# Performance work log

Hardware: AMD Instinct MI355X
Metric: run time of the kernel (lower is better)

The kernel has to match this reference:

```python
import jax, jax.numpy as jnp
import numpy as np

B, S, D = 2, 2048, 1024
H, HD = 16, 64  # H*HD == D (required by proj layer)
SCALE = D ** -0.5  # NOTE: original scales by full input dim (x.shape[-1]), not head dim


def setup_inputs() -> dict:
    key = jax.random.key(0)
    ks = jax.random.split(key, 7)
    std = D ** -0.5
    x = jax.random.normal(ks[0], (B, S, D), dtype=jnp.float32)
    # per-head projection weights, stacked: [H, D, HD] so x @ Wq[h] == Linear(D->HD)
    Wq = jax.random.normal(ks[1], (H, D, HD), dtype=jnp.float32) * std
    Wk = jax.random.normal(ks[2], (H, D, HD), dtype=jnp.float32) * std
    Wv = jax.random.normal(ks[3], (H, D, HD), dtype=jnp.float32) * std
    # output projection Linear(D, D) with bias
    Wp = jax.random.normal(ks[4], (D, D), dtype=jnp.float32) * std
    bp = jax.random.normal(ks[5], (D,), dtype=jnp.float32) * 0.01
    return {"x": x, "Wq": Wq, "Wk": Wk, "Wv": Wv, "Wp": Wp, "bp": bp}


def reference(x, Wq, Wk, Wv, Wp, bp):
    # All heads see the full x (atsp=False path). Dropout in eval mode (identity).
    q = jnp.einsum('bsd,hde->bhse', x, Wq)  # [B,H,S,HD]
    k = jnp.einsum('bsd,hde->bhse', x, Wk)
    v = jnp.einsum('bsd,hde->bhse', x, Wv)
    scores = jnp.einsum('bhse,bhte->bhst', q, k) * SCALE  # [B,H,S,S]
    causal = jnp.tril(jnp.ones((S, S), dtype=bool))
    scores = jnp.where(causal, scores, -jnp.inf)
    attn = jax.nn.softmax(scores, axis=-1)
    out = jnp.einsum('bhst,bhte->bhse', attn, v)          # [B,H,S,HD]
    # concat heads along last dim in head order: [B,S,H*HD]
    out = out.transpose(0, 2, 1, 3).reshape(B, S, H * HD)
    return out @ Wp.T + bp
```

## Files before the change

kernel.cpp:

```cpp
#include <hip/hip_runtime.h>

typedef __bf16 bf16x8 __attribute__((ext_vector_type(8)));
typedef __bf16 bf16x4 __attribute__((ext_vector_type(4)));
typedef float f32x4 __attribute__((ext_vector_type(4)));
typedef unsigned short u16;
typedef unsigned int u32;

static constexpr int kS = 2048, kD = 1024, kHD = 64;
static constexpr float kQScale = 0.03125f * 1.44269504f;

__device__ __forceinline__ u16 f2bf(float f) {
  union { float f; u32 u; } v; v.f = f;
  u32 r = v.u + 0x7FFFu + ((v.u >> 16) & 1u);
  return (u16)(r >> 16);
}
__device__ __forceinline__ float bf2f(u16 u) {
  union { u32 u; float f; } v; v.u = ((u32)u) << 16;
  return v.f;
}
__device__ __forceinline__ u32 pk2(float a, float b) {
  return (u32)f2bf(a) | ((u32)f2bf(b) << 16);
}
__device__ __forceinline__ f32x4 mfma16(bf16x8 a, bf16x8 b, f32x4 c) {
  return __builtin_amdgcn_mfma_f32_16x16x32_bf16(a, b, c, 0, 0, 0);
}
__device__ __forceinline__ void gld16(u16* lds, const u16* g) {
  __builtin_amdgcn_global_load_lds(
      (const __attribute__((address_space(1))) u32*)g,
      (__attribute__((address_space(3))) u32*)lds, 16, 0, 0);
}

__device__ __forceinline__ bool probe_f32(const u16* __restrict__ xr) {
  int ex = (xr[threadIdx.x] >> 7) & 0xFF;
  int n = __syncthreads_count(ex >= 134);
  return n > 8;
}

union Pack8 { u16 u[8]; uint4 v; };

__global__ void cast_all_kernel(const void* Wq, const void* Wk, const void* Wv,
                                const void* Wp, const void* x,
                                u16* __restrict__ Wt, u16* __restrict__ Wpb,
                                u16* __restrict__ xb) {
  bool f32m = probe_f32((const u16*)x);
  int bid = blockIdx.x;
  int t = threadIdx.x;
  __shared__ float Ts[64][65];
  if (bid < 768) {
    int u = bid >> 4;
    int d0 = (bid & 15) * 64;
    int w = u >> 4, h = u & 15;
    const void* srcv = (w == 0) ? Wq : (w == 1) ? Wk : Wv;
    const float* sf = (const float*)srcv + (size_t)h * kD * kHD;
    const u16*   sb = (const u16*)srcv + (size_t)h * kD * kHD;
    int row = t >> 4;
    int c4 = (t & 15) * 4;
    for (int rr = 0; rr < 64; rr += 16) {
      int r = rr + row;
      if (f32m) {
        float4 v = *(const float4*)&sf[(size_t)(d0 + r) * kHD + c4];
        Ts[r][c4 + 0] = v.x; Ts[r][c4 + 1] = v.y; Ts[r][c4 + 2] = v.z; Ts[r][c4 + 3] = v.w;
      } else {
        const u16* p = &sb[(size_t)(d0 + r) * kHD + c4];
        Ts[r][c4 + 0] = bf2f(p[0]); Ts[r][c4 + 1] = bf2f(p[1]);
        Ts[r][c4 + 2] = bf2f(p[2]); Ts[r][c4 + 3] = bf2f(p[3]);
      }
    }
    __syncthreads();
    for (int rr = 0; rr < 64; rr += 16) {
      int e = rr + row;
      uint2 pk;
      pk.x = pk2(Ts[c4 + 0][e], Ts[c4 + 1][e]);
      pk.y = pk2(Ts[c4 + 2][e], Ts[c4 + 3][e]);
      *(uint2*)&Wt[(size_t)u * (kHD * kD) + (size_t)e * kD + d0 + c4] = pk;
    }
  } else if (bid < 1792) {
    if (!f32m) return;
    int i = ((bid - 768) * 256 + t) * 4;
    float4 v = *(const float4*)((const float*)Wp + i);
    uint2 pk; pk.x = pk2(v.x, v.y); pk.y = pk2(v.z, v.w);
    *(uint2*)&Wpb[i] = pk;
  } else {
    if (!f32m) return;
    size_t i = ((size_t)(bid - 1792) * 256 + t) * 8;
    const float* xf = (const float*)x;
    float4 a = *(const float4*)&xf[i];
    float4 b = *(const float4*)&xf[i + 4];
    Pack8 pk;
    pk.u[0] = f2bf(a.x); pk.u[1] = f2bf(a.y); pk.u[2] = f2bf(a.z); pk.u[3] = f2bf(a.w);
    pk.u[4] = f2bf(b.x); pk.u[5] = f2bf(b.y); pk.u[6] = f2bf(b.z); pk.u[7] = f2bf(b.w);
    *(uint4*)&xb[i] = pk.v;
  }
}

__global__ __launch_bounds__(256) void qkv_gemm_kernel(const u16* __restrict__ xb,
    const u16* __restrict__ Wt, u16* __restrict__ Q, u16* __restrict__ K,
    u16* __restrict__ Vt, const void* __restrict__ x) {
  bool f32m = probe_f32((const u16*)x);
  const u16* xsrc = f32m ? xb : (const u16*)x;
  int m0 = blockIdx.x * 128;
  int n0 = blockIdx.y * 128;
  int w = (int)(blockIdx.y >> 3);
  const u16 *Ap, *Bp; int a0, b0;
  if (w == 2) { Ap = xsrc; a0 = m0; Bp = Wt; b0 = n0; }
  else        { Ap = Wt; a0 = n0; Bp = xsrc; b0 = m0; }
  int t = threadIdx.x;
  int wv = t >> 6, l = t & 63;
  int fr = l & 15, fq = l >> 4;
  int wI = (wv >> 1) * 64, wJ = (wv & 1) * 64;
  __shared__ __align__(16) u16 As[128][64];
  __shared__ __align__(16) u16 Bs[128][64];
  int srow = l >> 3;
  int scol = (((l & 7) ^ srow)) * 8;
  int dcol = (l & 7) * 8;
  int sw = fr & 7;
  f32x4 acc[4][4];
#pragma unroll
  for (int ii = 0; ii < 4; ++ii)
#pragma unroll
    for (int jj = 0; jj < 4; ++jj)
      for (int i = 0; i < 4; ++i) acc[ii][jj][i] = 0.f;

  for (int kb = 0; kb < kD / 64; ++kb) {
    int k0 = kb * 64;
    __syncthreads();
#pragma unroll
    for (int j = 0; j < 4; ++j) {
      int row = (wv * 4 + j) * 8 + srow;
      gld16(&As[row][dcol], &Ap[(size_t)(a0 + row) * kD + k0 + scol]);
      gld16(&Bs[row][dcol], &Bp[(size_t)(b0 + row) * kD + k0 + scol]);
    }
    __syncthreads();
    bf16x8 af[4][2], bg[4][2];
#pragma unroll
    for (int ii = 0; ii < 4; ++ii) {
      af[ii][0] = *(const bf16x8*)&As[wI + ii * 16 + fr][((0 + fq) ^ sw) * 8];
      af[ii][1] = *(const bf16x8*)&As[wI + ii * 16 + fr][((4 + fq) ^ sw) * 8];
    }
#pragma unroll
    for (int jj = 0; jj < 4; ++jj) {
      bg[jj][0] = *(const bf16x8*)&Bs[wJ + jj * 16 + fr][((0 + fq) ^ sw) * 8];
      bg[jj][1] = *(const bf16x8*)&Bs[wJ + jj * 16 + fr][((4 + fq) ^ sw) * 8];
    }
#pragma unroll
    for (int ii = 0; ii < 4; ++ii)
#pragma unroll
      for (int jj = 0; jj < 4; ++jj) {
        acc[ii][jj] = mfma16(af[ii][0], bg[jj][0], acc[ii][jj]);
        acc[ii][jj] = mfma16(af[ii][1], bg[jj][1], acc[ii][jj]);
      }
  }

  if (w == 2) {
    int uh = wv & 1;
    int u = 2 * blockIdx.y + uh;
    int h = u & 15;
#pragma unroll
    for (int jj = 0; jj < 4; ++jj) {
      int e = jj * 16 + fr;
#pragma unroll
      for (int ii = 0; ii < 4; ++ii) {
        int m = m0 + wI + ii * 16 + fq * 4;
        int b = m >> 11, s0 = m & 2047;
        int bh = b * 16 + h;
        *(bf16x4*)&Vt[((size_t)bh * kHD + e) * kS + s0] =
            __builtin_convertvector(acc[ii][jj], bf16x4);
      }
    }
  } else {
    int uh = wv >> 1;
    int u = 2 * blockIdx.y + uh;
    int h = u & 15;
    bool isQ = (w == 0);
    u16* dst = isQ ? Q : K;
#pragma unroll
    for (int jj = 0; jj < 4; ++jj) {
      int m = m0 + wJ + jj * 16 + fr;
      int b = m >> 11, s = m & 2047;
      int bh = b * 16 + h;
      size_t rowb = ((size_t)bh * kS + s) * kHD;
#pragma unroll
      for (int ii = 0; ii < 4; ++ii) {
        int e0 = ii * 16 + fq * 4;
        f32x4 v = acc[ii][jj];
        if (isQ) v *= kQScale;
        *(bf16x4*)&dst[rowb + e0] = __builtin_convertvector(v, bf16x4);
      }
    }
  }
}

static __device__ const signed char kQtab[48] = {
  15,31,30,31,
  14,29,28,30,29,
  13,27,26,28,27,
  12,25,24,26,25,
  11,23,22,24,23,
  10,21,20,22,21,
   9,19,18,20,19,
   8,17,16,18,17,
   7,16,
   6,5,4,3,2,1,0};
static __device__ const signed char kPtab[48] = {
  2,0,0,1,
  2,0,0,1,1,
  2,0,0,1,1,
  2,0,0,1,1,
  2,0,0,1,1,
  2,0,0,1,1,
  2,0,0,1,1,
  2,0,0,1,1,
  2,1,
  2,2,2,2,2,2,2};

__global__ __launch_bounds__(256) void attn_kernel(const u16* __restrict__ Q,
    const u16* __restrict__ K, const u16* __restrict__ Vt, u16* __restrict__ cat,
    float* __restrict__ Po, float* __restrict__ Pl, int split) {
  int bh = (int)(blockIdx.x & 31);
  int c  = (int)(blockIdx.x >> 5);
  int qb, part;
  if (split) { qb = kQtab[c]; part = kPtab[c]; }
  else       { qb = 31 - c;   part = 2; }
  int h0 = (qb + 2) >> 1;
  int tbeg = (part == 1) ? h0 : 0;
  int tend = (part == 0) ? h0 - 1 : qb;
  int q0 = qb * 64;
  int t = threadIdx.x;
  int wv = t >> 6, l = t & 63;
  int fr = l & 15, fq = l >> 4;
  __shared__ __align__(16) u16 Ks[64][64];
  __shared__ __align__(16) u16 Vs[64][64];
  __shared__ __align__(16) u16 Ps[4][16][64];
  const u16* Qb = Q + (size_t)bh * kS * kHD;
  const u16* Kb = K + (size_t)bh * kS * kHD;
  const u16* Vb = Vt + (size_t)bh * kHD * kS;

  int qrow = q0 + wv * 16 + fr;
  bf16x8 qf0 = *(const bf16x8*)&Qb[(size_t)qrow * kHD + fq * 8];
  bf16x8 qf1 = *(const bf16x8*)&Qb[(size_t)qrow * kHD + 32 + fq * 8];

  f32x4 O[4];
#pragma unroll
  for (int nt = 0; nt < 4; ++nt) for (int i = 0; i < 4; ++i) O[nt][i] = 0.f;
  float lsum = 0.f;

  int jr = l >> 3;
  int dcol = (l & 7) * 8;
  int scol = ((l & 7) ^ jr) * 8;
  int r0 = wv * 16 + jr;
  int r1 = r0 + 8;
  int sw = fr & 7;

  {
    int tb = tbeg * 64;
    gld16(&Ks[r0][dcol], &Kb[(size_t)(tb + r0) * kHD + scol]);
    gld16(&Ks[r1][dcol], &Kb[(size_t)(tb + r1) * kHD + scol]);
    gld16(&Vs[r0][dcol], &Vb[(size_t)r0 * kS + tb + scol]);
    gld16(&Vs[r1][dcol], &Vb[(size_t)r1 * kS + tb + scol]);
  }
  __syncthreads();

  for (int tt = tbeg; tt <= tend; ++tt) {
    int t0 = tt * 64;
    f32x4 sc[4];
    __builtin_amdgcn_s_setprio(1);
#pragma unroll
    for (int nt = 0; nt < 4; ++nt) {
      f32x4 z; z[0] = z[1] = z[2] = z[3] = 0.f;
      bf16x8 a0 = *(const bf16x8*)&Ks[nt * 16 + fr][((0 + fq) ^ sw) * 8];
      bf16x8 a1 = *(const bf16x8*)&Ks[nt * 16 + fr][((4 + fq) ^ sw) * 8];
      z = mfma16(a0, qf0, z);
      z = mfma16(a1, qf1, z);
      sc[nt] = z;
    }
    __builtin_amdgcn_s_setprio(0);
    if (tt == qb) {
#pragma unroll
      for (int nt = 0; nt < 4; ++nt)
#pragma unroll
        for (int r = 0; r < 4; ++r)
          if (t0 + nt * 16 + fq * 4 + r > qrow) sc[nt][r] = -__builtin_inff();
    }
#pragma unroll
    for (int nt = 0; nt < 4; ++nt) {
#pragma unroll
      for (int r = 0; r < 4; ++r) {
        float p = exp2f(sc[nt][r]);
        sc[nt][r] = p;
        lsum += p;
      }
      *(bf16x4*)&Ps[wv][fr][(((nt * 2 + (fq >> 1)) ^ sw) * 8) + (fq & 1) * 4] =
          __builtin_convertvector(sc[nt], bf16x4);
    }
    bf16x8 pf0 = *(const bf16x8*)&Ps[wv][fr][(fq ^ sw) * 8];
    bf16x8 pf1 = *(const bf16x8*)&Ps[wv][fr][((4 + fq) ^ sw) * 8];
    __builtin_amdgcn_s_setprio(1);
#pragma unroll
    for (int nt = 0; nt < 4; ++nt) {
      bf16x8 v0 = *(const bf16x8*)&Vs[nt * 16 + fr][((0 + fq) ^ sw) * 8];
      bf16x8 v1 = *(const bf16x8*)&Vs[nt * 16 + fr][((4 + fq) ^ sw) * 8];
      O[nt] = mfma16(v0, pf0, O[nt]);
      O[nt] = mfma16(v1, pf1, O[nt]);
    }
    __builtin_amdgcn_s_setprio(0);
    if (tt < tend) {
      __syncthreads();
      int t0n = t0 + 64;
      gld16(&Ks[r0][dcol], &Kb[(size_t)(t0n + r0) * kHD + scol]);
      gld16(&Ks[r1][dcol], &Kb[(size_t)(t0n + r1) * kHD + scol]);
      gld16(&Vs[r0][dcol], &Vb[(size_t)r0 * kS + t0n + scol]);
      gld16(&Vs[r1][dcol], &Vb[(size_t)r1 * kS + t0n + scol]);
      __syncthreads();
    }
  }
  lsum += __shfl_xor(lsum, 16, 64);
  lsum += __shfl_xor(lsum, 32, 64);
  if (part == 2) {
    float inv = 1.0f / lsum;
    int b = bh >> 4, h = bh & 15;
    size_t rowbase = ((size_t)(b * kS + qrow)) * kD + h * kHD;
#pragma unroll
    for (int nt = 0; nt < 4; ++nt) {
      f32x4 ov = O[nt] * inv;
      *(bf16x4*)&cat[rowbase + nt * 16 + fq * 4] = __builtin_convertvector(ov, bf16x4);
    }
  } else {
    int slot = ((bh << 4) + (qb - 16)) * 2 + part;
    float* Pb = Po + (size_t)slot * 4096 + (wv * 16 + fr) * 64;
    if (fq == 0) Pl[slot * 64 + wv * 16 + fr] = lsum;
#pragma unroll
    for (int nt = 0; nt < 4; ++nt)
      *(f32x4*)&Pb[nt * 16 + fq * 4] = O[nt];
  }
}

__global__ __launch_bounds__(256) void attn_combine_kernel(
    const float* __restrict__ Po, const float* __restrict__ Pl,
    u16* __restrict__ cat) {
  int bh = (int)(blockIdx.x >> 4);
  int lvl = (int)(blockIdx.x & 15);
  int t = threadIdx.x;
  int slot = ((bh << 4) + lvl) * 2;
  int b = bh >> 4, h = bh & 15;
  int e0 = (t & 15) * 4;
  for (int qq = 0; qq < 64; qq += 16) {
    int q = qq + (t >> 4);
    const float* A = Po + (size_t)slot * 4096 + q * 64 + e0;
    float l = Pl[slot * 64 + q] + Pl[(slot + 1) * 64 + q];
    float inv = 1.0f / l;
    f32x4 a = *(const f32x4*)A;
    f32x4 bv = *(const f32x4*)(A + 4096);
    f32x4 v = (a + bv) * inv;
    int qrow = (lvl + 16) * 64 + q;
    *(bf16x4*)&cat[((size_t)(b * kS + qrow)) * kD + h * kHD + e0] =
        __builtin_convertvector(v, bf16x4);
  }
}

__global__ __launch_bounds__(256) void out_gemm_kernel(const u16* __restrict__ cat,
    const u16* __restrict__ Wpb, const void* __restrict__ Wp,
    const void* __restrict__ bp, void* __restrict__ out,
    const void* __restrict__ x) {
  bool f32m = probe_f32((const u16*)x);
  const u16* wsrc = f32m ? Wpb : (const u16*)Wp;
  int m0 = blockIdx.x * 64;
  int n0 = blockIdx.y * 128;
  int t = threadIdx.x;
  int wv = t >> 6, l = t & 63;
  int fr = l & 15, fq = l >> 4;
  int wI = (wv >> 1) * 64, wJ = (wv & 1) * 32;
  __shared__ __align__(16) u16 As[128][64];
  __shared__ __align__(16) u16 Bs[64][64];
  int srow = l >> 3;
  int scol = (((l & 7) ^ srow)) * 8;
  int dcol = (l & 7) * 8;
  int sw = fr & 7;
  f32x4 acc[4][2];
#pragma unroll
  for (int ii = 0; ii < 4; ++ii)
#pragma unroll
    for (int jj = 0; jj < 2; ++jj)
      for (int i = 0; i < 4; ++i) acc[ii][jj][i] = 0.f;

  for (int kb = 0; kb < kD / 64; ++kb) {
    int k0 = kb * 64;
    __syncthreads();
#pragma unroll
    for (int j = 0; j < 4; ++j) {
      int row = j * 32 + wv * 8 + srow;
      gld16(&As[row][dcol], &wsrc[(size_t)(n0 + row) * kD + k0 + scol]);
    }
#pragma unroll
    for (int j = 0; j < 2; ++j) {
      int row = j * 32 + wv * 8 + srow;
      gld16(&Bs[row][dcol], &cat[(size_t)(m0 + row) * kD + k0 + scol]);
    }
    __syncthreads();
    bf16x8 af[4][2], bg[2][2];
#pragma unroll
    for (int ii = 0; ii < 4; ++ii) {
      af[ii][0] = *(const bf16x8*)&As[wI + ii * 16 + fr][((0 + fq) ^ sw) * 8];
      af[ii][1] = *(const bf16x8*)&As[wI + ii * 16 + fr][((4 + fq) ^ sw) * 8];
    }
#pragma unroll
    for (int jj = 0; jj < 2; ++jj) {
      bg[jj][0] = *(const bf16x8*)&Bs[wJ + jj * 16 + fr][((0 + fq) ^ sw) * 8];
      bg[jj][1] = *(const bf16x8*)&Bs[wJ + jj * 16 + fr][((4 + fq) ^ sw) * 8];
    }
#pragma unroll
    for (int ii = 0; ii < 4; ++ii)
#pragma unroll
      for (int jj = 0; jj < 2; ++jj) {
        acc[ii][jj] = mfma16(af[ii][0], bg[jj][0], acc[ii][jj]);
        acc[ii][jj] = mfma16(af[ii][1], bg[jj][1], acc[ii][jj]);
      }
  }
  const float* bpf = (const float*)bp;
  const u16*   bpb = (const u16*)bp;
#pragma unroll
  for (int ii = 0; ii < 4; ++ii) {
    int n = n0 + wI + ii * 16 + fq * 4;
    f32x4 bias;
    if (f32m) bias = *(const f32x4*)&bpf[n];
    else { bias[0] = bf2f(bpb[n]); bias[1] = bf2f(bpb[n + 1]);
           bias[2] = bf2f(bpb[n + 2]); bias[3] = bf2f(bpb[n + 3]); }
#pragma unroll
    for (int jj = 0; jj < 2; ++jj) {
      int m = m0 + wJ + jj * 16 + fr;
      f32x4 v = acc[ii][jj] + bias;
      if (f32m) *(f32x4*)&((float*)out)[(size_t)m * kD + n] = v;
      else      *(bf16x4*)&((u16*)out)[(size_t)m * kD + n] = __builtin_convertvector(v, bf16x4);
    }
  }
}

extern "C" void kernel_launch(void* const* d_in, const int* in_sizes, int n_in,
                              void* d_out, int out_size, void* d_ws, size_t ws_size,
                              hipStream_t stream) {
  const void* x  = d_in[0];
  const void* Wq = d_in[1];
  const void* Wk = d_in[2];
  const void* Wv = d_in[3];
  const void* Wp = d_in[4];
  const void* bp = d_in[5];

  char* ws = (char*)d_ws;
  u16* Wt  = (u16*)(ws + 256);
  u16* Wpb = (u16*)(ws + 256 + 6291456);
  u16* Qp  = (u16*)(ws + 256 + 6291456 + 2097152);
  u16* Kp  = Qp  + (size_t)32 * 2048 * 64;
  u16* Vtp = Kp  + (size_t)32 * 2048 * 64;
  u16* xb  = Vtp + (size_t)32 * 2048 * 64;
  u16* cat = xb;
  size_t poOff = 256 + 6291456 + 2097152 + (size_t)4 * 8388608;
  size_t plOff = poOff + (size_t)32 * 16 * 2 * 4096 * 4;
  size_t needWs = plOff + (size_t)32 * 16 * 2 * 64 * 4;
  int split = (ws_size >= needWs) ? 1 : 0;
  float* Po = (float*)(ws + poOff);
  float* Pl = (float*)(ws + plOff);

  cast_all_kernel<<<3840, 256, 0, stream>>>(Wq, Wk, Wv, Wp, x, Wt, Wpb, xb);
  qkv_gemm_kernel<<<dim3(32, 24), 256, 0, stream>>>(xb, Wt, Qp, Kp, Vtp, x);
  attn_kernel<<<split ? 1536 : 1024, 256, 0, stream>>>(Qp, Kp, Vtp, cat, Po, Pl, split);
  if (split)
    attn_combine_kernel<<<512, 256, 0, stream>>>(Po, Pl, cat);
  out_gemm_kernel<<<dim3(64, 8), 256, 0, stream>>>(cat, Wpb, Wp, bp, d_out, x);
}
```

Baseline: 181.1 us.

## Process two query sub-tiles per wave in attention with 128-thread blocks

Restructures the attention kernel so each of 2 waves handles 32 query rows (two 16-row groups) instead of 4 waves handling 16 rows each. Each K/V fragment loaded from shared memory is reused across both query groups, halving LDS reads per MFMA, and each thread issues twice as many global loads to fill the tiles. The trade-off is fewer waves per block to hide latency, roughly double the accumulator registers per thread, and lower per-block parallelism.

Measured after the change: 186.2 us. +2.8%, slower.

```diff
diff --git a/kernel.cpp b/kernel.cpp
--- a/kernel.cpp
+++ b/kernel.cpp
@@ -213,7 +213,7 @@
   2,1,
   2,2,2,2,2,2,2};
 
-__global__ __launch_bounds__(256) void attn_kernel(const u16* __restrict__ Q,
+__global__ __launch_bounds__(128) void attn_kernel(const u16* __restrict__ Q,
     const u16* __restrict__ K, const u16* __restrict__ Vt, u16* __restrict__ cat,
     float* __restrict__ Po, float* __restrict__ Pl, int split) {
   int bh = (int)(blockIdx.x & 31);
@@ -230,107 +230,141 @@
   int fr = l & 15, fq = l >> 4;
   __shared__ __align__(16) u16 Ks[64][64];
   __shared__ __align__(16) u16 Vs[64][64];
-  __shared__ __align__(16) u16 Ps[4][16][64];
+  __shared__ __align__(16) u16 Ps[2][2][16][64];
   const u16* Qb = Q + (size_t)bh * kS * kHD;
   const u16* Kb = K + (size_t)bh * kS * kHD;
   const u16* Vb = Vt + (size_t)bh * kHD * kS;
 
-  int qrow = q0 + wv * 16 + fr;
-  bf16x8 qf0 = *(const bf16x8*)&Qb[(size_t)qrow * kHD + fq * 8];
-  bf16x8 qf1 = *(const bf16x8*)&Qb[(size_t)qrow * kHD + 32 + fq * 8];
-
-  f32x4 O[4];
-#pragma unroll
-  for (int nt = 0; nt < 4; ++nt) for (int i = 0; i < 4; ++i) O[nt][i] = 0.f;
-  float lsum = 0.f;
-
-  int jr = l >> 3;
-  int dcol = (l & 7) * 8;
-  int scol = ((l & 7) ^ jr) * 8;
-  int r0 = wv * 16 + jr;
-  int r1 = r0 + 8;
+  int qrow[2];
+  bf16x8 qf[2][2];
+#pragma unroll
+  for (int g = 0; g < 2; ++g) {
+    qrow[g] = q0 + wv * 32 + g * 16 + fr;
+    qf[g][0] = *(const bf16x8*)&Qb[(size_t)qrow[g] * kHD + fq * 8];
+    qf[g][1] = *(const bf16x8*)&Qb[(size_t)qrow[g] * kHD + 32 + fq * 8];
+  }
+
+  f32x4 O[2][4];
+#pragma unroll
+  for (int g = 0; g < 2; ++g)
+#pragma unroll
+    for (int nt = 0; nt < 4; ++nt)
+      for (int i = 0; i < 4; ++i) O[g][nt][i] = 0.f;
+  float lsum[2] = {0.f, 0.f};
+
+  int jr = t >> 3;
+  int dcol = (t & 7) * 8;
+  int scol = ((t & 7) ^ (jr & 7)) * 8;
   int sw = fr & 7;
 
   {
     int tb = tbeg * 64;
-    gld16(&Ks[r0][dcol], &Kb[(size_t)(tb + r0) * kHD + scol]);
-    gld16(&Ks[r1][dcol], &Kb[(size_t)(tb + r1) * kHD + scol]);
-    gld16(&Vs[r0][dcol], &Vb[(size_t)r0 * kS + tb + scol]);
-    gld16(&Vs[r1][dcol], &Vb[(size_t)r1 * kS + tb + scol]);
+#pragma unroll
+    for (int k = 0; k < 4; ++k) {
+      int r = jr + k * 16;
+      gld16(&Ks[r][dcol], &Kb[(size_t)(tb + r) * kHD + scol]);
+      gld16(&Vs[r][dcol], &Vb[(size_t)r * kS + tb + scol]);
+    }
   }
   __syncthreads();
 
   for (int tt = tbeg; tt <= tend; ++tt) {
     int t0 = tt * 64;
-    f32x4 sc[4];
+    f32x4 sc[2][4];
     __builtin_amdgcn_s_setprio(1);
 #pragma unroll
     for (int nt = 0; nt < 4; ++nt) {
-      f32x4 z; z[0] = z[1] = z[2] = z[3] = 0.f;
       bf16x8 a0 = *(const bf16x8*)&Ks[nt * 16 + fr][((0 + fq) ^ sw) * 8];
       bf16x8 a1 = *(const bf16x8*)&Ks[nt * 16 + fr][((4 + fq) ^ sw) * 8];
-      z = mfma16(a0, qf0, z);
-      z = mfma16(a1, qf1, z);
-      sc[nt] = z;
+#pragma unroll
+      for (int g = 0; g < 2; ++g) {
+        f32x4 z; z[0] = z[1] = z[2] = z[3] = 0.f;
+        z = mfma16(a0, qf[g][0], z);
+        z = mfma16(a1, qf[g][1], z);
+        sc[g][nt] = z;
+      }
     }
     __builtin_amdgcn_s_setprio(0);
     if (tt == qb) {
 #pragma unroll
-      for (int nt = 0; nt < 4; ++nt)
-#pragma unroll
-        for (int r = 0; r < 4; ++r)
-          if (t0 + nt * 16 + fq * 4 + r > qrow) sc[nt][r] = -__builtin_inff();
-    }
-#pragma unroll
-    for (int nt = 0; nt < 4; ++nt) {
-#pragma unroll
-      for (int r = 0; r < 4; ++r) {
-        float p = exp2f(sc[nt][r]);
-        sc[nt][r] = p;
-        lsum += p;
-      }
-      *(bf16x4*)&Ps[wv][fr][(((nt * 2 + (fq >> 1)) ^ sw) * 8) + (fq & 1) * 4] =
-          __builtin_convertvector(sc[nt], bf16x4);
-    }
-    bf16x8 pf0 = *(const bf16x8*)&Ps[wv][fr][(fq ^ sw) * 8];
-    bf16x8 pf1 = *(const bf16x8*)&Ps[wv][fr][((4 + fq) ^ sw) * 8];
+      for (int g = 0; g < 2; ++g)
+#pragma unroll
+        for (int nt = 0; nt < 4; ++nt)
+#pragma unroll
+          for (int r = 0; r < 4; ++r)
+            if (t0 + nt * 16 + fq * 4 + r > qrow[g]) sc[g][nt][r] = -__builtin_inff();
+    }
+#pragma unroll
+    for (int g = 0; g < 2; ++g)
+#pragma unroll
+      for (int nt = 0; nt < 4; ++nt) {
+#pragma unroll
+        for (int r = 0; r < 4; ++r) {
+          float p = exp2f(sc[g][nt][r]);
+          sc[g][nt][r] = p;
+          lsum[g] += p;
+        }
+        *(bf16x4*)&Ps[wv][g][fr][(((nt * 2 + (fq >> 1)) ^ sw) * 8) + (fq & 1) * 4] =
+            __builtin_convertvector(sc[g][nt], bf16x4);
+      }
+    bf16x8 pf[2][2];
+#pragma unroll
+    for (int g = 0; g < 2; ++g) {
+      pf[g][0] = *(const bf16x8*)&Ps[wv][g][fr][(fq ^ sw) * 8];
+      pf[g][1] = *(const bf16x8*)&Ps[wv][g][fr][((4 + fq) ^ sw) * 8];
+    }
     __builtin_amdgcn_s_setprio(1);
 #pragma unroll
     for (int nt = 0; nt < 4; ++nt) {
       bf16x8 v0 = *(const bf16x8*)&Vs[nt * 16 + fr][((0 + fq) ^ sw) * 8];
       bf16x8 v1 = *(const bf16x8*)&Vs[nt * 16 + fr][((4 + fq) ^ sw) * 8];
-      O[nt] = mfma16(v0, pf0, O[nt]);
-      O[nt] = mfma16(v1, pf1, O[nt]);
+#pragma unroll
+      for (int g = 0; g < 2; ++g) {
+        O[g][nt] = mfma16(v0, pf[g][0], O[g][nt]);
+        O[g][nt] = mfma16(v1, pf[g][1], O[g][nt]);
+      }
     }
     __builtin_amdgcn_s_setprio(0);
     if (tt < tend) {
       __syncthreads();
       int t0n = t0 + 64;
-      gld16(&Ks[r0][dcol], &Kb[(size_t)(t0n + r0) * kHD + scol]);
-      gld16(&Ks[r1][dcol], &Kb[(size_t)(t0n + r1) * kHD + scol]);
-      gld16(&Vs[r0][dcol], &Vb[(size_t)r0 * kS + t0n + scol]);
-      gld16(&Vs[r1][dcol], &Vb[(size_t)r1 * kS + t0n + scol]);
+#pragma unroll
+      for (int k = 0; k < 4; ++k) {
+        int r = jr + k * 16;
+        gld16(&Ks[r][dcol], &Kb[(size_t)(t0n + r) * kHD + scol]);
+        gld16(&Vs[r][dcol], &Vb[(size_t)r * kS + t0n + scol]);
+      }
       __syncthreads();
     }
   }
-  lsum += __shfl_xor(lsum, 16, 64);
-  lsum += __shfl_xor(lsum, 32, 64);
+#pragma unroll
+  for (int g = 0; g < 2; ++g) {
+    lsum[g] += __shfl_xor(lsum[g], 16, 64);
+    lsum[g] += __shfl_xor(lsum[g], 32, 64);
+  }
   if (part == 2) {
-    float inv = 1.0f / lsum;
     int b = bh >> 4, h = bh & 15;
-    size_t rowbase = ((size_t)(b * kS + qrow)) * kD + h * kHD;
-#pragma unroll
-    for (int nt = 0; nt < 4; ++nt) {
-      f32x4 ov = O[nt] * inv;
-      *(bf16x4*)&cat[rowbase + nt * 16 + fq * 4] = __builtin_convertvector(ov, bf16x4);
+#pragma unroll
+    for (int g = 0; g < 2; ++g) {
+      float inv = 1.0f / lsum[g];
+      size_t rowbase = ((size_t)(b * kS + qrow[g])) * kD + h * kHD;
+#pragma unroll
+      for (int nt = 0; nt < 4; ++nt) {
+        f32x4 ov = O[g][nt] * inv;
+        *(bf16x4*)&cat[rowbase + nt * 16 + fq * 4] = __builtin_convertvector(ov, bf16x4);
+      }
     }
   } else {
     int slot = ((bh << 4) + (qb - 16)) * 2 + part;
-    float* Pb = Po + (size_t)slot * 4096 + (wv * 16 + fr) * 64;
-    if (fq == 0) Pl[slot * 64 + wv * 16 + fr] = lsum;
-#pragma unroll
-    for (int nt = 0; nt < 4; ++nt)
-      *(f32x4*)&Pb[nt * 16 + fq * 4] = O[nt];
+#pragma unroll
+    for (int g = 0; g < 2; ++g) {
+      int q = wv * 32 + g * 16 + fr;
+      float* Pb = Po + (size_t)slot * 4096 + q * 64;
+      if (fq == 0) Pl[slot * 64 + q] = lsum[g];
+#pragma unroll
+      for (int nt = 0; nt < 4; ++nt)
+        *(f32x4*)&Pb[nt * 16 + fq * 4] = O[g][nt];
+    }
   }
 }
 
@@ -461,7 +495,7 @@
 
   cast_all_kernel<<<3840, 256, 0, stream>>>(Wq, Wk, Wv, Wp, x, Wt, Wpb, xb);
   qkv_gemm_kernel<<<dim3(32, 24), 256, 0, stream>>>(xb, Wt, Qp, Kp, Vtp, x);
-  attn_kernel<<<split ? 1536 : 1024, 256, 0, stream>>>(Qp, Kp, Vtp, cat, Po, Pl, split);
+  attn_kernel<<<split ? 1536 : 1024, 128, 0, stream>>>(Qp, Kp, Vtp, cat, Po, Pl, split);
   if (split)
     attn_combine_kernel<<<512, 256, 0, stream>>>(Po, Pl, cat);
   out_gemm_kernel<<<dim3(64, 8), 256, 0, stream>>>(cat, Wpb, Wp, bp, d_out, x);
```
